# Kernel tuning notes

Hardware: AMD Instinct MI355X
Metric: run time of the kernel (lower is better)

The kernel has to match this reference:

```python
import jax, jax.numpy as jnp
import numpy as np
import math

H = 16          # num_heads
DN = 128        # qk_nope_head_dim
DR = 64         # qk_rope_head_dim
DV = 128        # v_head_dim
Q_LORA = 1536
KV_LORA = 512
EPS = 1e-6
ROPE_BASE = 10000.0
YARN_FACTOR = 16.0
ORIG_MAX = 8192


def rmsnorm(x, w):
    return x * jax.lax.rsqrt(jnp.mean(x * x, axis=-1, keepdims=True) + EPS) * w


def rotate_half(x):
    h = x.shape[-1] // 2
    return jnp.concatenate([-x[..., h:], x[..., :h]], axis=-1)


def yarn_cos_sin(L, dtype):
    # YaRN-scaled inverse frequencies (RotaryEmbedding defaults)
    pos2 = jnp.arange(0, DR, 2, dtype=jnp.float32)
    inv_freq = 1.0 / (ROPE_BASE ** (pos2 / DR))
    wavelen = 2.0 * jnp.pi / inv_freq
    # low_freq_factor=1.0, high_freq_factor=4.0
    ramp = jnp.clip((ORIG_MAX / wavelen - 1.0) / (4.0 - 1.0), 0.0, 1.0)
    inv_freq = inv_freq * (1.0 - ramp) + (inv_freq / YARN_FACTOR) * ramp
    t = jnp.arange(L, dtype=jnp.float32)
    freqs = jnp.outer(t, inv_freq)                      # [L, DR/2]
    emb = jnp.concatenate([freqs, freqs], axis=-1)      # [L, DR]
    attn_factor = 0.1 * math.log(YARN_FACTOR) + 1.0     # yarn attention scaling
    cos = (jnp.cos(emb) * attn_factor)[None, :, None, :].astype(dtype)
    sin = (jnp.sin(emb) * attn_factor)[None, :, None, :].astype(dtype)
    return cos, sin


def setup_inputs() -> dict:
    key = jax.random.key(0)
    ks = jax.random.split(key, 8)
    s = 0.02
    hid = 2048
    return {
        "x": jax.random.normal(ks[0], (2, 2048, hid), jnp.float32),
        "w_qa": jax.random.normal(ks[1], (hid, Q_LORA), jnp.float32) * s,
        "q_norm_w": jnp.ones((Q_LORA,), jnp.float32),
        "w_qb": jax.random.normal(ks[2], (Q_LORA, H * (DN + DR)), jnp.float32) * s,
        "w_kva": jax.random.normal(ks[3], (hid, KV_LORA + DR), jnp.float32) * s,
        "kv_norm_w": jnp.ones((KV_LORA,), jnp.float32),
        "w_kvb": jax.random.normal(ks[4], (KV_LORA, H * (DN + DV)), jnp.float32) * s,
        "w_o": jax.random.normal(ks[5], (H * DV, hid), jnp.float32) * s,
    }


def reference(x, w_qa, q_norm_w, w_qb, w_kva, kv_norm_w, w_kvb, w_o):
    B, L, _ = x.shape
    # --- low-rank Q path ---
    q = rmsnorm(x @ w_qa, q_norm_w) @ w_qb               # [B, L, H*(DN+DR)]
    q = q.reshape(B, L, H, DN + DR)
    q_nope, q_rope = q[..., :DN], q[..., DN:]
    # --- low-rank KV path ---
    kv = x @ w_kva                                       # [B, L, KV_LORA+DR]
    kv_c, k_rope = kv[..., :KV_LORA], kv[..., KV_LORA:]
    kv = rmsnorm(kv_c, kv_norm_w) @ w_kvb                # [B, L, H*(DN+DV)]
    kv = kv.reshape(B, L, H, DN + DV)
    k_nope, v = kv[..., :DN], kv[..., DN:]
    k_rope = jnp.broadcast_to(k_rope[:, :, None, :], (B, L, H, DR))
    # --- decoupled RoPE on rope sub-dims ---
    cos, sin = yarn_cos_sin(L, x.dtype)
    q_rope = q_rope * cos + rotate_half(q_rope) * sin
    k_rope = k_rope * cos + rotate_half(k_rope) * sin
    q = jnp.concatenate([q_nope, q_rope], axis=-1)       # [B, L, H, DN+DR]
    k = jnp.concatenate([k_nope, k_rope], axis=-1)
    # --- causal SDPA, scale = 1/sqrt(qk head dim) ---
    scale = 1.0 / math.sqrt(DN + DR)
    scores = jnp.einsum('blhd,bmhd->bhlm', q, k) * scale
    mask = jnp.tril(jnp.ones((L, L), bool))
    scores = jnp.where(mask[None, None], scores, jnp.array(-1e30, scores.dtype))
    attn = jax.nn.softmax(scores, axis=-1)
    out = jnp.einsum('bhlm,bmhd->blhd', attn, v)         # [B, L, H, DV]
    return out.reshape(B, L, H * DV) @ w_o               # [B, L, hidden]
```

## Files before the change

kernel.cpp:

```cpp
#include <hip/hip_runtime.h>
#include <hip/hip_bf16.h>
#include <math.h>

#define H_    16
#define B_    2
#define L_    2048
#define HID_  2048
#define QL_   1536
#define KVL_  512

typedef unsigned short u16;
typedef __attribute__((ext_vector_type(8))) short bf16x8;
typedef __attribute__((ext_vector_type(4))) float f32x4;

__device__ __forceinline__ float bf2f(u16 u) {
    unsigned int x = ((unsigned int)u) << 16;
    return __uint_as_float(x);
}
__device__ __forceinline__ u16 f2bf(float f) {
    __hip_bfloat16 b = __float2bfloat16(f);
    return *(u16*)&b;
}
__device__ __forceinline__ void g2l16(const void* g, void* l) {
    __builtin_amdgcn_global_load_lds(
        (const __attribute__((address_space(1))) unsigned int*)g,
        (__attribute__((address_space(3))) unsigned int*)l,
        16, 0, 0);
}
__device__ __forceinline__ int kswz(int l, int d) {
    return (((d >> 3) ^ (l & 7)) << 3) | (d & 7);
}

#define QSCALE (0.07216878364870323f * 1.4426950408889634f)

__device__ inline void yarn_cs(int l, int j, float& c, float& s)
{
    float invf = expf(-(float)(2 * j) * (9.210340371976184f / 64.f));
    float wavelen = 6.283185307179586f / invf;
    float ramp = (8192.f / wavelen - 1.f) * (1.f / 3.f);
    ramp = fminf(fmaxf(ramp, 0.f), 1.f);
    float invf2 = invf * (1.f - ramp) + invf * (1.f / 16.f) * ramp;
    float ang = (float)l * invf2;
    const float af = 1.2772588722239781f;
    c = cosf(ang) * af;
    s = sinf(ang) * af;
}

__global__ __launch_bounds__(256) void frontend(
    const float* __restrict__ x, u16* __restrict__ x_b,
    const float* __restrict__ w_qa, const float* __restrict__ w_kva,
    const float* __restrict__ w_qb, const float* __restrict__ w_kvb,
    const float* __restrict__ w_o,
    u16* __restrict__ Wt_qa, u16* __restrict__ Wt_kva, u16* __restrict__ Wt_qb,
    u16* __restrict__ Wt_kvb, u16* __restrict__ Wt_o,
    const float* __restrict__ qnw, const float* __restrict__ kvnw,
    float* __restrict__ tab)
{
    __shared__ float t[64][65];
    int bid = blockIdx.x;
    if (bid >= 7840) {
        int idx = (bid - 7840) * 256 + threadIdx.x;
        int l = idx >> 5, j = idx & 31;
        float c, s; yarn_cs(l, j, c, s);
        tab[l * 64 + j] = c;
        tab[l * 64 + 32 + j] = s;
        return;
    }
    if (bid >= 3744) {
        int idx = (bid - 3744) * 256 + threadIdx.x;
        float4 a = ((const float4*)x)[idx * 2];
        float4 b = ((const float4*)x)[idx * 2 + 1];
        union { uint4 v; u16 s[8]; } u;
        u.s[0] = f2bf(a.x); u.s[1] = f2bf(a.y); u.s[2] = f2bf(a.z); u.s[3] = f2bf(a.w);
        u.s[4] = f2bf(b.x); u.s[5] = f2bf(b.y); u.s[6] = f2bf(b.z); u.s[7] = f2bf(b.w);
        ((uint4*)x_b)[idx] = u.v;
        return;
    }
    const float* W; u16* Wt; int K, N; const float* wvec = nullptr; int loc;
    if (bid < 768)       { W = w_qa;  Wt = Wt_qa;  K = 2048; N = 1536; loc = bid; }
    else if (bid < 1056) { W = w_kva; Wt = Wt_kva; K = 2048; N = 576;  loc = bid - 768; }
    else if (bid < 2208) { W = w_qb;  Wt = Wt_qb;  K = 1536; N = 3072; wvec = qnw;  loc = bid - 1056; }
    else if (bid < 2720) { W = w_kvb; Wt = Wt_kvb; K = 512;  N = 4096; wvec = kvnw; loc = bid - 2208; }
    else                 { W = w_o;   Wt = Wt_o;   K = 2048; N = 2048; loc = bid - 2720; }
    const int nx = N >> 6;
    const int n0 = (loc % nx) * 64, k0 = (loc / nx) * 64;
    const int tid = threadIdx.x;
    {
        int lr = tid >> 2, nc = (tid & 3) * 16;
        float wk = wvec ? wvec[k0 + lr] : 1.f;
        const float* src = W + (size_t)(k0 + lr) * N + n0 + nc;
#pragma unroll
        for (int j = 0; j < 16; j += 4) {
            float4 v = *(const float4*)(src + j);
            t[lr][nc + j] = v.x * wk; t[lr][nc + j + 1] = v.y * wk;
            t[lr][nc + j + 2] = v.z * wk; t[lr][nc + j + 3] = v.w * wk;
        }
    }
    __syncthreads();
    {
        int nr = tid >> 2, kc = (tid & 3) * 16;
        union { uint4 v[2]; u16 s[16]; } u;
#pragma unroll
        for (int j = 0; j < 16; ++j) u.s[j] = f2bf(t[kc + j][nr]);
        uint4* dst = (uint4*)(Wt + (size_t)(n0 + nr) * K + k0 + kc);
        dst[0] = u.v[0]; dst[1] = u.v[1];
    }
}

__global__ __launch_bounds__(256) void rowss2(
    const u16* __restrict__ qaR, const u16* __restrict__ kvf,
    float* __restrict__ sc_q, float* __restrict__ sc_kv)
{
    __shared__ float red[4];
    int row = blockIdx.x;
    const u16* ir; int ncols; float* outp;
    if (row < 4096) { ir = qaR + (size_t)row * 1536; ncols = 1536; outp = sc_q + row; }
    else { row -= 4096; ir = kvf + (size_t)row * 576; ncols = 512; outp = sc_kv + row; }
    const int tid = threadIdx.x;
    const int nch = ncols >> 3;
    float ss = 0.f;
    for (int c = tid; c < nch; c += 256) {
        union { uint4 v; u16 s[8]; } u;
        u.v = *(const uint4*)(ir + c * 8);
#pragma unroll
        for (int j = 0; j < 8; ++j) { float v = bf2f(u.s[j]); ss += v * v; }
    }
#pragma unroll
    for (int o = 32; o > 0; o >>= 1) ss += __shfl_xor(ss, o);
    if ((tid & 63) == 0) red[tid >> 6] = ss;
    __syncthreads();
    if (tid == 0) {
        float tot = red[0] + red[1] + red[2] + red[3];
        *outp = rsqrtf(tot / (float)ncols + 1e-6f);
    }
}

template<int NI> struct EpiStoreF32 {
    float* C; int ldc;
    __device__ void operator()(const f32x4* acc, int m0, int n0, int wr, int wc,
                               int g, int n) const {
#pragma unroll
        for (int mi = 0; mi < 4; ++mi)
#pragma unroll
            for (int ni = 0; ni < NI; ++ni)
#pragma unroll
                for (int i = 0; i < 4; ++i)
                    C[(size_t)(m0 + wr + mi * 16 + g * 4 + i) * ldc
                      + n0 + wc + ni * 16 + n] = acc[mi * NI + ni][i];
    }
};
struct EpiQA {
    u16* qaR; u16* kvf;
    __device__ void operator()(const f32x4* acc, int m0, int n0, int wr, int wc,
                               int g, int n) const {
        int c0 = n0 + wc;
#pragma unroll
        for (int mi = 0; mi < 4; ++mi)
#pragma unroll
            for (int i = 0; i < 4; ++i) {
                int rr = m0 + wr + mi * 16 + g * 4 + i;
#pragma unroll
                for (int ni = 0; ni < 4; ++ni) {
                    int c = c0 + ni * 16 + n;
                    float v = acc[mi * 4 + ni][i];
                    if (c < 1536)      qaR[(size_t)rr * 1536 + c] = f2bf(v);
                    else if (c < 2112) kvf[(size_t)rr * 576 + (c - 1536)] = f2bf(v);
                }
            }
    }
};
struct EpiQ {
    u16* Qb; const float* tab; const float* sc;
    __device__ void operator()(const f32x4* acc, int m0, int n0, int wr, int wc,
                               int g, int n) const {
        int c0 = n0 + wc;
        int h = c0 / 192, r0 = c0 % 192;
#pragma unroll
        for (int mi = 0; mi < 4; ++mi)
#pragma unroll
            for (int i = 0; i < 4; ++i) {
                int rr = m0 + wr + mi * 16 + g * 4 + i;
                int b = rr >> 11, l = rr & 2047;
                float scl = sc[rr] * QSCALE;
                size_t base = ((size_t)(b * 16 + h) * 2048 + l) * 192;
                if (r0 < 128) {
#pragma unroll
                    for (int ni = 0; ni < 4; ++ni)
                        Qb[base + r0 + ni * 16 + n] = f2bf(acc[mi * 4 + ni][i] * scl);
                } else {
#pragma unroll
                    for (int ni = 0; ni < 2; ++ni) {
                        int j = ni * 16 + n;
                        float cs = tab[l * 64 + j], sn = tab[l * 64 + 32 + j];
                        float lo = acc[mi * 4 + ni][i] * scl;
                        float hi = acc[mi * 4 + ni + 2][i] * scl;
                        Qb[base + 128 + j] = f2bf(lo * cs - hi * sn);
                        Qb[base + 160 + j] = f2bf(hi * cs + lo * sn);
                    }
                }
            }
    }
};
struct EpiKV {
    u16* Kb; u16* Vc; const float* sc;
    __device__ void operator()(const f32x4* acc, int m0, int n0, int wr, int wc,
                               int g, int n) const {
        int c0 = n0 + wc;
        int h = c0 >> 8, r0 = c0 & 255;
#pragma unroll
        for (int mi = 0; mi < 4; ++mi)
#pragma unroll
            for (int i = 0; i < 4; ++i) {
                int rr = m0 + wr + mi * 16 + g * 4 + i;
                int b = rr >> 11, l = rr & 2047;
                float scl = sc[rr];
                if (r0 < 128) {
                    size_t base = ((size_t)(b * 16 + h) * 2048 + l) * 192;
#pragma unroll
                    for (int ni = 0; ni < 4; ++ni) {
                        int d = r0 + ni * 16 + n;
                        Kb[base + kswz(l, d)] = f2bf(acc[mi * 4 + ni][i] * scl);
                    }
                } else {
#pragma unroll
                    for (int ni = 0; ni < 4; ++ni)
                        Vc[(size_t)rr * 2048 + h * 128 + (r0 - 128) + ni * 16 + n]
                            = f2bf(acc[mi * 4 + ni][i] * scl);
                }
            }
    }
};

template<class Epi>
__device__ __forceinline__ void gemm_body(
    u16* As, u16* Bs,
    const u16* __restrict__ A, int lda,
    const u16* __restrict__ Bt, int ldb,
    int K, Epi epi, int lin, int nwg, int nx)
{
    const int tid = threadIdx.x;
    const int w = tid >> 6, lane = tid & 63;
    const int g = lane >> 4, n = lane & 15;
    const int wr = (w >> 1) * 64, wc = (w & 1) * 64;
    const int swz = (lin & 7) * (nwg >> 3) + (lin >> 3);
    const int m0 = (swz / nx) * 128, n0 = (swz % nx) * 128;
    const int arow = lane >> 2;
    const int acol = (((lane & 3) ^ ((lane >> 3) & 3)) * 8);
    const int rsw = (n >> 1) & 3;

    f32x4 acc[4][4];
#pragma unroll
    for (int mi = 0; mi < 4; ++mi)
#pragma unroll
        for (int ni = 0; ni < 4; ++ni) acc[mi][ni] = (f32x4){0.f, 0.f, 0.f, 0.f};

    for (int k0 = 0; k0 < K; k0 += 32) {
        __syncthreads();
#pragma unroll
        for (int i = 0; i < 2; ++i) {
            int seg = w * 2 + i;
            int row = seg * 16 + arow;
            g2l16(A + (size_t)(m0 + row) * lda + k0 + acol, &As[seg * 512]);
        }
#pragma unroll
        for (int i = 0; i < 2; ++i) {
            int seg = w * 2 + i;
            int row = seg * 16 + arow;
            g2l16(Bt + (size_t)(n0 + row) * ldb + k0 + acol, &Bs[seg * 512]);
        }
        __syncthreads();

        bf16x8 af[4], bf[4];
#pragma unroll
        for (int mi = 0; mi < 4; ++mi)
            af[mi] = *(const bf16x8*)&As[(wr + mi * 16 + n) * 32 + ((g ^ rsw) << 3)];
#pragma unroll
        for (int ni = 0; ni < 4; ++ni)
            bf[ni] = *(const bf16x8*)&Bs[(wc + ni * 16 + n) * 32 + ((g ^ rsw) << 3)];
#pragma unroll
        for (int mi = 0; mi < 4; ++mi)
#pragma unroll
            for (int ni = 0; ni < 4; ++ni)
                acc[mi][ni] = __builtin_amdgcn_mfma_f32_16x16x32_bf16(
                    af[mi], bf[ni], acc[mi][ni], 0, 0, 0);
    }
    epi(&acc[0][0], m0, n0, wr, wc, g, n);
}

template<class Epi>
__global__ __launch_bounds__(256) void gemm_bf16(
    const u16* __restrict__ A, int lda,
    const u16* __restrict__ Bt, int ldb,
    int K, Epi epi, int nx)
{
    __shared__ u16 As[128 * 32];
    __shared__ u16 Bs[128 * 32];
    gemm_body<Epi>(As, Bs, A, lda, Bt, ldb, K, epi, blockIdx.x, gridDim.x, nx);
}

__global__ __launch_bounds__(256) void gemm_qkv(
    const u16* __restrict__ qaR, const u16* __restrict__ Wt_qb, EpiQ eq,
    const u16* __restrict__ kvf, const u16* __restrict__ Wt_kvb, EpiKV ekv)
{
    __shared__ u16 As[128 * 32];
    __shared__ u16 Bs[128 * 32];
    int bid = blockIdx.x;
    if (bid < 768)
        gemm_body<EpiQ>(As, Bs, qaR, 1536, Wt_qb, 1536, 1536, eq, bid, 768, 24);
    else
        gemm_body<EpiKV>(As, Bs, kvf, 576, Wt_kvb, 512, 512, ekv, bid - 768, 1024, 32);
}

__global__ __launch_bounds__(256) void krope_vtrans(
    const u16* __restrict__ kvf_b, u16* __restrict__ Kb,
    const float* __restrict__ tab,
    const u16* __restrict__ Vc, u16* __restrict__ Vt)
{
    __shared__ u16 t[64][72];
    int bid = blockIdx.x;
    if (bid < 8192) {
        int idx = bid * 256 + threadIdx.x;
        int j = idx & 31;
        int l = (idx >> 5) & 2047;
        int bh = idx >> 16;
        int b = bh >> 4;
        size_t row = (size_t)(b * 2048 + l);
        float x0 = bf2f(kvf_b[row * 576 + 512 + j]);
        float x1 = bf2f(kvf_b[row * 576 + 544 + j]);
        float cs = tab[l * 64 + j], sn = tab[l * 64 + 32 + j];
        size_t base = ((size_t)bh * 2048 + l) * 192;
        Kb[base + kswz(l, 128 + j)] = f2bf(x0 * cs - x1 * sn);
        Kb[base + kswz(l, 160 + j)] = f2bf(x1 * cs + x0 * sn);
        return;
    }
    int vb = bid - 8192;
    const int bh = vb & 31, b = bh >> 4, h = bh & 15;
    const int dv0 = ((vb >> 5) & 1) * 64;
    const int l0 = (vb >> 6) * 64;
    const int tid = threadIdx.x;
    {
        int lr = tid >> 2, dc = (tid & 3) * 16;
        const u16* src = Vc + (size_t)(b * 2048 + l0 + lr) * 2048 + h * 128 + dv0 + dc;
        uint4 v0 = *(const uint4*)src;
        uint4 v1 = *(const uint4*)(src + 8);
        *(uint4*)&t[lr][dc] = v0;
        *(uint4*)&t[lr][dc + 8] = v1;
    }
    __syncthreads();
    {
        int dvr = tid >> 2, lc = (tid & 3) * 16;
        union { uint4 v[2]; u16 s[16]; } u;
#pragma unroll
        for (int j = 0; j < 16; ++j) u.s[j] = t[lc + j][dvr];
        uint4* dst = (uint4*)(Vt + ((size_t)bh * 128 + dv0 + dvr) * 2048 + l0 + lc);
        dst[0] = u.v[0]; dst[1] = u.v[1];
    }
}

__global__ __launch_bounds__(256) void attn_mfma(
    const u16* __restrict__ Qb,
    const u16* __restrict__ Kb,
    const u16* __restrict__ Vt,
    u16* __restrict__ outp)
{
    __shared__ u16 Kl[64 * 192];
    __shared__ u16 Vl[128 * 64];

    const int tid = threadIdx.x;
    const int w = tid >> 6, lane = tid & 63;
    const int g = lane >> 4, n = lane & 15;
    const int n7 = n & 7;
    const int lin = blockIdx.x;
    const int xcd = lin & 7, j = lin >> 3;
    const int qt = 31 - (j >> 2);
    const int bh = xcd * 4 + (j & 3);
    const int b = bh >> 4;
    const int qb0 = qt << 6;

    u16* PtW = Kl + w * 1280;

    const u16* KsrcBase = Kb + (size_t)bh * L_ * 192;
    const u16* VsrcBase = Vt + (size_t)bh * 128 * 2048;

    bf16x8 qf[6];
    {
        const int qrow = qb0 + w * 16 + n;
        const u16* qp = Qb + ((size_t)bh * L_ + qrow) * 192 + g * 8;
#pragma unroll
        for (int kk = 0; kk < 6; ++kk)
            qf[kk] = *(const bf16x8*)(qp + kk * 32);
    }

    f32x4 acc[8];
#pragma unroll
    for (int dt = 0; dt < 8; ++dt) acc[dt] = (f32x4){0.f, 0.f, 0.f, 0.f};
    float li[4] = {0.f, 0.f, 0.f, 0.f};

    const int ntiles = qt + 1;
    for (int kt = 0; kt < ntiles; ++kt) {
        const int kb = kt << 6;
        __syncthreads();
        {
            const u16* Ksrc = KsrcBase + (size_t)kb * 192;
#pragma unroll
            for (int i = 0; i < 6; ++i) {
                int c = i * 4 + w;
                g2l16(Ksrc + c * 512 + lane * 8, &Kl[c * 512]);
            }
        }
        {
#pragma unroll
            for (int i = 0; i < 4; ++i) {
                int c = i * 4 + w;
                int dv = c * 8 + (lane >> 3);
                int blk = (lane & 7) ^ (lane >> 3);
                g2l16(VsrcBase + (size_t)dv * 2048 + kb + blk * 8, &Vl[c * 512]);
            }
        }
        __syncthreads();

        f32x4 s[4];
#pragma unroll
        for (int c = 0; c < 4; ++c) s[c] = (f32x4){0.f, 0.f, 0.f, 0.f};
        __builtin_amdgcn_s_setprio(1);
#pragma unroll
        for (int c = 0; c < 4; ++c)
#pragma unroll
            for (int kk = 0; kk < 6; ++kk) {
                bf16x8 kf = *(const bf16x8*)
                    &Kl[(c * 16 + n) * 192 + ((kk * 4 + g) ^ n7) * 8];
                s[c] = __builtin_amdgcn_mfma_f32_16x16x32_bf16(qf[kk], kf, s[c], 0, 0, 0);
            }
        __builtin_amdgcn_s_setprio(0);

        const bool diag = (kt == qt);
#pragma unroll
        for (int i = 0; i < 4; ++i) {
            float v[4];
            if (diag) {
                int qr = qb0 + w * 16 + g * 4 + i;
#pragma unroll
                for (int c = 0; c < 4; ++c)
                    v[c] = (kb + c * 16 + n <= qr) ? s[c][i] : -1e30f;
            } else {
#pragma unroll
                for (int c = 0; c < 4; ++c) v[c] = s[c][i];
            }
            float p0 = __builtin_amdgcn_exp2f(v[0]);
            float p1 = __builtin_amdgcn_exp2f(v[1]);
            float p2 = __builtin_amdgcn_exp2f(v[2]);
            float p3 = __builtin_amdgcn_exp2f(v[3]);
            li[i] += (p0 + p1) + (p2 + p3);
            s[0][i] = p0; s[1][i] = p1; s[2][i] = p2; s[3][i] = p3;
        }

        __syncthreads();

#pragma unroll
        for (int c = 0; c < 4; ++c) {
            union { double d; u16 hh[4]; } u;
#pragma unroll
            for (int i = 0; i < 4; ++i) u.hh[i] = f2bf(s[c][i]);
            *(double*)&PtW[(c * 16 + n) * 20 + g * 4] = u.d;
        }
        asm volatile("s_waitcnt lgkmcnt(0)" ::: "memory");
        __builtin_amdgcn_sched_barrier(0);

        union { bf16x8 v; short e[8]; } pf[2];
#pragma unroll
        for (int ks = 0; ks < 2; ++ks)
#pragma unroll
            for (int jj = 0; jj < 8; ++jj)
                pf[ks].e[jj] = *(const short*)&PtW[(ks * 32 + g * 8 + jj) * 20 + n];

        __builtin_amdgcn_s_setprio(1);
#pragma unroll
        for (int dt = 0; dt < 8; ++dt) {
#pragma unroll
            for (int ks = 0; ks < 2; ++ks) {
                bf16x8 vf = *(const bf16x8*)
                    &Vl[(dt * 16 + n) * 64 + (((ks * 4 + g) ^ n7) << 3)];
                acc[dt] = __builtin_amdgcn_mfma_f32_16x16x32_bf16(pf[ks].v, vf, acc[dt], 0, 0, 0);
            }
        }
        __builtin_amdgcn_s_setprio(0);
    }

    float inv[4];
#pragma unroll
    for (int i = 0; i < 4; ++i) {
        float t = li[i];
        t += __shfl_xor(t, 1);
        t += __shfl_xor(t, 2);
        t += __shfl_xor(t, 4);
        t += __shfl_xor(t, 8);
        inv[i] = __frcp_rn(t);
    }
#pragma unroll
    for (int dt = 0; dt < 8; ++dt) {
#pragma unroll
        for (int i = 0; i < 4; ++i) {
            int qr = qb0 + w * 16 + g * 4 + i;
            outp[(size_t)(b * L_ + qr) * 2048 + (bh & 15) * 128 + dt * 16 + n]
                = f2bf(acc[dt][i] * inv[i]);
        }
    }
}

extern "C" void kernel_launch(void* const* d_in, const int* in_sizes, int n_in,
                              void* d_out, int out_size, void* d_ws, size_t ws_size,
                              hipStream_t stream)
{
    const float* x     = (const float*)d_in[0];
    const float* w_qa  = (const float*)d_in[1];
    const float* qnw   = (const float*)d_in[2];
    const float* w_qb  = (const float*)d_in[3];
    const float* w_kva = (const float*)d_in[4];
    const float* kvnw  = (const float*)d_in[5];
    const float* w_kvb = (const float*)d_in[6];
    const float* w_o   = (const float*)d_in[7];
    float* out = (float*)d_out;
    u16* W = (u16*)d_ws;

    const size_t o_wt_qa  = 0;
    const size_t o_wt_qb  = (size_t)2176 * 2048;
    const size_t o_wt_kvb = o_wt_qb  + (size_t)3072 * 1536;
    const size_t o_wt_o   = o_wt_kvb + (size_t)4096 * 512;
    const size_t o_tab    = o_wt_o   + (size_t)2048 * 2048;
    const size_t o_sc     = o_tab    + 262144;
    const size_t o_Qb     = o_sc     + 16384;
    const size_t o_Kb     = o_Qb     + 12582912;
    const size_t o_Vt     = o_Kb     + 12582912;
    const size_t o_Vc     = o_Vt     + 8388608;
    const size_t o_xb     = o_Vc     + 8388608;

    u16* Wt_qa  = W + o_wt_qa;
    u16* Wt_kva = W + o_wt_qa + (size_t)1536 * 2048;
    u16* Wt_qb  = W + o_wt_qb;
    u16* Wt_kvb = W + o_wt_kvb;
    u16* Wt_o   = W + o_wt_o;
    float* tab  = (float*)(W + o_tab);
    float* sc_q  = (float*)(W + o_sc);
    float* sc_kv = sc_q + 4096;
    u16* Qb     = W + o_Qb;
    u16* qaR_b  = W + o_Kb;
    u16* Kb     = W + o_Kb;
    u16* kvf_b  = W + o_Vt;
    u16* Vt     = W + o_Vt;
    u16* Vc     = W + o_Vc;
    u16* atto_b = W + o_Vc;
    u16* x_b    = W + o_xb;

    dim3 blk(256);

    frontend<<<8096, blk, 0, stream>>>(
        x, x_b, w_qa, w_kva, w_qb, w_kvb, w_o,
        Wt_qa, Wt_kva, Wt_qb, Wt_kvb, Wt_o, qnw, kvnw, tab);

    gemm_bf16<EpiQA><<<544, blk, 0, stream>>>(
        x_b, 2048, Wt_qa, 2048, 2048, EpiQA{qaR_b, kvf_b}, 17);
    rowss2<<<8192, blk, 0, stream>>>(qaR_b, kvf_b, sc_q, sc_kv);
    gemm_qkv<<<1792, blk, 0, stream>>>(
        qaR_b, Wt_qb, EpiQ{Qb, tab, sc_q},
        kvf_b, Wt_kvb, EpiKV{Kb, Vc, sc_kv});
    krope_vtrans<<<10240, blk, 0, stream>>>(kvf_b, Kb, tab, Vc, Vt);

    attn_mfma<<<dim3(1024), blk, 0, stream>>>(Qb, Kb, Vt, atto_b);
    gemm_bf16<EpiStoreF32<4>><<<512, blk, 0, stream>>>(
        atto_b, 2048, Wt_o, 2048, 2048, EpiStoreF32<4>{out, 2048}, 16);
}
```

Before: 294.2 us.

## Fuse K-rope into rowss kernel and write V transposed from GEMM epilogue

Removes the separate krope_vtrans kernel. The rotary embedding on the shared k_rope is now computed inside the RMS row-sum kernel for KV rows and written to all heads, and the KV GEMM epilogue writes V directly in transposed [bh, dv, l] layout with packed 4-element stores. This drops a kernel launch plus the round trip of V through an intermediate buffer. Workspace buffers are reassigned to avoid aliasing, since Kb and Vt are now written earlier. The transposed epilogue stores are 8-byte strided writes, which may coalesce less well than the old row-major ones.

```diff
diff --git a/kernel.cpp b/kernel.cpp
--- a/kernel.cpp
+++ b/kernel.cpp
@@ -107,15 +107,16 @@
     }
 }
 
-__global__ __launch_bounds__(256) void rowss2(
+__global__ __launch_bounds__(256) void rowss2k(
     const u16* __restrict__ qaR, const u16* __restrict__ kvf,
-    float* __restrict__ sc_q, float* __restrict__ sc_kv)
+    float* __restrict__ sc_q, float* __restrict__ sc_kv,
+    u16* __restrict__ Kb, const float* __restrict__ tab)
 {
     __shared__ float red[4];
     int row = blockIdx.x;
-    const u16* ir; int ncols; float* outp;
+    const u16* ir; int ncols; float* outp; bool isKV = false;
     if (row < 4096) { ir = qaR + (size_t)row * 1536; ncols = 1536; outp = sc_q + row; }
-    else { row -= 4096; ir = kvf + (size_t)row * 576; ncols = 512; outp = sc_kv + row; }
+    else { row -= 4096; ir = kvf + (size_t)row * 576; ncols = 512; outp = sc_kv + row; isKV = true; }
     const int tid = threadIdx.x;
     const int nch = ncols >> 3;
     float ss = 0.f;
@@ -132,6 +133,24 @@
     if (tid == 0) {
         float tot = red[0] + red[1] + red[2] + red[3];
         *outp = rsqrtf(tot / (float)ncols + 1e-6f);
+    }
+    if (isKV) {
+        int j = tid & 31;
+        int h2 = tid >> 5;
+        int l = row & 2047, b = row >> 11;
+        float x0 = bf2f(ir[512 + j]);
+        float x1 = bf2f(ir[544 + j]);
+        float cs = tab[l * 64 + j], sn = tab[l * 64 + 32 + j];
+        u16 ra = f2bf(x0 * cs - x1 * sn);
+        u16 rb = f2bf(x1 * cs + x0 * sn);
+        int ka = kswz(l, 128 + j), kb2 = kswz(l, 160 + j);
+#pragma unroll
+        for (int hh = 0; hh < 2; ++hh) {
+            int h = h2 + hh * 8;
+            size_t base = ((size_t)(b * 16 + h) * 2048 + l) * 192;
+            Kb[base + ka]  = ra;
+            Kb[base + kb2] = rb;
+        }
     }
 }
 
@@ -202,32 +221,46 @@
     }
 };
 struct EpiKV {
-    u16* Kb; u16* Vc; const float* sc;
+    u16* Kb; u16* Vt; const float* sc;
     __device__ void operator()(const f32x4* acc, int m0, int n0, int wr, int wc,
                                int g, int n) const {
         int c0 = n0 + wc;
         int h = c0 >> 8, r0 = c0 & 255;
-#pragma unroll
-        for (int mi = 0; mi < 4; ++mi)
-#pragma unroll
-            for (int i = 0; i < 4; ++i) {
-                int rr = m0 + wr + mi * 16 + g * 4 + i;
-                int b = rr >> 11, l = rr & 2047;
-                float scl = sc[rr];
-                if (r0 < 128) {
+        if (r0 < 128) {
+#pragma unroll
+            for (int mi = 0; mi < 4; ++mi)
+#pragma unroll
+                for (int i = 0; i < 4; ++i) {
+                    int rr = m0 + wr + mi * 16 + g * 4 + i;
+                    int b = rr >> 11, l = rr & 2047;
+                    float scl = sc[rr];
                     size_t base = ((size_t)(b * 16 + h) * 2048 + l) * 192;
 #pragma unroll
                     for (int ni = 0; ni < 4; ++ni) {
                         int d = r0 + ni * 16 + n;
                         Kb[base + kswz(l, d)] = f2bf(acc[mi * 4 + ni][i] * scl);
                     }
-                } else {
-#pragma unroll
-                    for (int ni = 0; ni < 4; ++ni)
-                        Vc[(size_t)rr * 2048 + h * 128 + (r0 - 128) + ni * 16 + n]
-                            = f2bf(acc[mi * 4 + ni][i] * scl);
                 }
-            }
+        } else {
+            int b = m0 >> 11;
+            int lb0 = (m0 & 2047) + wr + g * 4;
+#pragma unroll
+            for (int mi = 0; mi < 4; ++mi) {
+                int lb = lb0 + mi * 16;
+                int rrb = m0 + wr + mi * 16 + g * 4;
+                float s0 = sc[rrb], s1 = sc[rrb + 1], s2 = sc[rrb + 2], s3 = sc[rrb + 3];
+#pragma unroll
+                for (int ni = 0; ni < 4; ++ni) {
+                    int dv = (r0 - 128) + ni * 16 + n;
+                    union { double d; u16 hh[4]; } u;
+                    u.hh[0] = f2bf(acc[mi * 4 + ni][0] * s0);
+                    u.hh[1] = f2bf(acc[mi * 4 + ni][1] * s1);
+                    u.hh[2] = f2bf(acc[mi * 4 + ni][2] * s2);
+                    u.hh[3] = f2bf(acc[mi * 4 + ni][3] * s3);
+                    *(double*)&Vt[((size_t)(b * 16 + h) * 128 + dv) * 2048 + lb] = u.d;
+                }
+            }
+        }
     }
 };
 
@@ -309,52 +342,6 @@
         gemm_body<EpiQ>(As, Bs, qaR, 1536, Wt_qb, 1536, 1536, eq, bid, 768, 24);
     else
         gemm_body<EpiKV>(As, Bs, kvf, 576, Wt_kvb, 512, 512, ekv, bid - 768, 1024, 32);
-}
-
-__global__ __launch_bounds__(256) void krope_vtrans(
-    const u16* __restrict__ kvf_b, u16* __restrict__ Kb,
-    const float* __restrict__ tab,
-    const u16* __restrict__ Vc, u16* __restrict__ Vt)
-{
-    __shared__ u16 t[64][72];
-    int bid = blockIdx.x;
-    if (bid < 8192) {
-        int idx = bid * 256 + threadIdx.x;
-        int j = idx & 31;
-        int l = (idx >> 5) & 2047;
-        int bh = idx >> 16;
-        int b = bh >> 4;
-        size_t row = (size_t)(b * 2048 + l);
-        float x0 = bf2f(kvf_b[row * 576 + 512 + j]);
-        float x1 = bf2f(kvf_b[row * 576 + 544 + j]);
-        float cs = tab[l * 64 + j], sn = tab[l * 64 + 32 + j];
-        size_t base = ((size_t)bh * 2048 + l) * 192;
-        Kb[base + kswz(l, 128 + j)] = f2bf(x0 * cs - x1 * sn);
-        Kb[base + kswz(l, 160 + j)] = f2bf(x1 * cs + x0 * sn);
-        return;
-    }
-    int vb = bid - 8192;
-    const int bh = vb & 31, b = bh >> 4, h = bh & 15;
-    const int dv0 = ((vb >> 5) & 1) * 64;
-    const int l0 = (vb >> 6) * 64;
-    const int tid = threadIdx.x;
-    {
-        int lr = tid >> 2, dc = (tid & 3) * 16;
-        const u16* src = Vc + (size_t)(b * 2048 + l0 + lr) * 2048 + h * 128 + dv0 + dc;
-        uint4 v0 = *(const uint4*)src;
-        uint4 v1 = *(const uint4*)(src + 8);
-        *(uint4*)&t[lr][dc] = v0;
-        *(uint4*)&t[lr][dc + 8] = v1;
-    }
-    __syncthreads();
-    {
-        int dvr = tid >> 2, lc = (tid & 3) * 16;
-        union { uint4 v[2]; u16 s[16]; } u;
-#pragma unroll
-        for (int j = 0; j < 16; ++j) u.s[j] = t[lc + j][dvr];
-        uint4* dst = (uint4*)(Vt + ((size_t)bh * 128 + dv0 + dvr) * 2048 + l0 + lc);
-        dst[0] = u.v[0]; dst[1] = u.v[1];
-    }
 }
 
 __global__ __launch_bounds__(256) void attn_mfma(
@@ -523,7 +510,7 @@
     u16* W = (u16*)d_ws;
 
     const size_t o_wt_qa  = 0;
-    const size_t o_wt_qb  = (size_t)2176 * 2048;
+    const size_t o_wt_qb  = o_wt_qa  + (size_t)2176 * 2048;
     const size_t o_wt_kvb = o_wt_qb  + (size_t)3072 * 1536;
     const size_t o_wt_o   = o_wt_kvb + (size_t)4096 * 512;
     const size_t o_tab    = o_wt_o   + (size_t)2048 * 2048;
@@ -531,8 +518,10 @@
     const size_t o_Qb     = o_sc     + 16384;
     const size_t o_Kb     = o_Qb     + 12582912;
     const size_t o_Vt     = o_Kb     + 12582912;
-    const size_t o_Vc     = o_Vt     + 8388608;
-    const size_t o_xb     = o_Vc     + 8388608;
+    const size_t o_qaR    = o_Vt     + 8388608;
+    const size_t o_kvf    = o_qaR    + 6291456;
+    const size_t o_atto   = o_kvf    + 2359296;
+    const size_t o_xb     = o_atto   + 8388608;
 
     u16* Wt_qa  = W + o_wt_qa;
     u16* Wt_kva = W + o_wt_qa + (size_t)1536 * 2048;
@@ -543,12 +532,11 @@
     float* sc_q  = (float*)(W + o_sc);
     float* sc_kv = sc_q + 4096;
     u16* Qb     = W + o_Qb;
-    u16* qaR_b  = W + o_Kb;
     u16* Kb     = W + o_Kb;
-    u16* kvf_b  = W + o_Vt;
     u16* Vt     = W + o_Vt;
-    u16* Vc     = W + o_Vc;
-    u16* atto_b = W + o_Vc;
+    u16* qaR_b  = W + o_qaR;
+    u16* kvf_b  = W + o_kvf;
+    u16* atto_b = W + o_atto;
     u16* x_b    = W + o_xb;
 
     dim3 blk(256);
@@ -559,11 +547,10 @@
 
     gemm_bf16<EpiQA><<<544, blk, 0, stream>>>(
         x_b, 2048, Wt_qa, 2048, 2048, EpiQA{qaR_b, kvf_b}, 17);
-    rowss2<<<8192, blk, 0, stream>>>(qaR_b, kvf_b, sc_q, sc_kv);
+    rowss2k<<<8192, blk, 0, stream>>>(qaR_b, kvf_b, sc_q, sc_kv, Kb, tab);
     gemm_qkv<<<1792, blk, 0, stream>>>(
         qaR_b, Wt_qb, EpiQ{Qb, tab, sc_q},
-        kvf_b, Wt_kvb, EpiKV{Kb, Vc, sc_kv});
-    krope_vtrans<<<10240, blk, 0, stream>>>(kvf_b, Kb, tab, Vc, Vt);
+        kvf_b, Wt_kvb, EpiKV{Kb, Vt, sc_kv});
 
     attn_mfma<<<dim3(1024), blk, 0, stream>>>(Qb, Kb, Vt, atto_b);
     gemm_bf16<EpiStoreF32<4>><<<512, blk, 0, stream>>>(
```

Measured after the change: 302.1 us. 1.03x slower.
